# Optimization experiments

Measured on AMD Instinct MI355X. Metric: run time of the kernel, lower is better.

## Reference

```python
import jax, jax.numpy as jnp
import numpy as np

N, D, H, C, E = 16384, 768, 768, 2, 20

def setup_inputs() -> dict:
    key = jax.random.key(0)
    k1, k2, k3, k4, k5, k6 = jax.random.split(key, 6)
    return {
        "embeddings": jax.random.normal(k1, (N, D), dtype=jnp.float32),
        "component_idx": jax.random.randint(k2, (N,), 0, E, dtype=jnp.int64),
        "W1": jax.random.normal(k3, (E, D, H), dtype=jnp.float32) * (1.0 / np.sqrt(D)),
        "b1": jnp.zeros((E, H), dtype=jnp.float32),
        "W2": jax.random.normal(k4, (E, H, C), dtype=jnp.float32) * (1.0 / np.sqrt(H)),
        "b2": jnp.zeros((E, C), dtype=jnp.float32),
    }

def reference(embeddings, component_idx, W1, b1, W2, b2):
    # Each token n goes through expert component_idx[n]:
    #   y = relu(x @ W1[e] + b1[e]) @ W2[e] + b2[e]
    # The torch module's mask/cat/argsort reassembly is mathematically a
    # per-token select of its own expert's output at the original position.
    # Dense-expert formulation (standard jax MoE fallback), then gather.
    h = jax.nn.relu(jnp.einsum('nd,edh->enh', embeddings, W1) + b1[:, None, :])  # [E,N,H]
    y = jnp.einsum('enh,ehc->enc', h, W2) + b2[:, None, :]                        # [E,N,C]
    n_idx = jnp.arange(embeddings.shape[0])
    return y[component_idx, n_idx]  # [N,C]
```

## Files before the change

### kernel.cpp

```cpp
#include <hip/hip_runtime.h>

#define N_D 768
#define N_H 768
#define N_C 2
#define N_E 20
#define MT 128
#define NT 128
#define BK 32
#define KT (N_D / BK)
#define MAX_TILES 160
#define NCOL (N_H / NT)
#define ROWB (N_D * 2)

typedef __attribute__((ext_vector_type(8))) short short8;
typedef __attribute__((ext_vector_type(4))) float f32x4;

__device__ __forceinline__ unsigned short f2bf(float f) {
  unsigned u = __builtin_bit_cast(unsigned, f);
  u += 0x7FFFu + ((u >> 16) & 1u);
  return (unsigned short)(u >> 16);
}

#define GLD_LDS16(gp, lp)                                                        \
  __builtin_amdgcn_global_load_lds(                                              \
      (const __attribute__((address_space(1))) void*)(gp),                       \
      (__attribute__((address_space(3))) void*)(lp), 16, 0, 0)


__global__ __launch_bounds__(256) void k_hist(const int* __restrict__ cidx,
                                              int* __restrict__ counts, int n) {
  __shared__ int lc[N_E];
  if (threadIdx.x < N_E) lc[threadIdx.x] = 0;
  __syncthreads();
  for (int i = blockIdx.x * blockDim.x + threadIdx.x; i < n;
       i += gridDim.x * blockDim.x) {
    int e = cidx[i];
    e = e < 0 ? 0 : (e >= N_E ? N_E - 1 : e);
    atomicAdd(&lc[e], 1);
  }
  __syncthreads();
  if (threadIdx.x < N_E) atomicAdd(&counts[threadIdx.x], lc[threadIdx.x]);
}

__global__ void k_scan(const int* __restrict__ counts, int* __restrict__ offsets,
                       int* __restrict__ cursor, int* __restrict__ tiles,
                       int* __restrict__ numTiles) {
  if (threadIdx.x == 0) {
    int run = 0, t = 0;
    for (int e = 0; e < N_E; ++e) {
      offsets[e] = run;
      cursor[e] = run;
      int nt = (counts[e] + MT - 1) / MT;
      for (int m = 0; m < nt && t < MAX_TILES; ++m) tiles[t++] = (e << 8) | m;
      run += counts[e];
    }
    *numTiles = t;
  }
}


#define SG_TOK 64

__global__ __launch_bounds__(256) void k_scatter_gather(
    const int* __restrict__ cidx, int* __restrict__ cursor,
    int* __restrict__ sorted, const float* __restrict__ emb,
    unsigned short* __restrict__ Xg, int n) {
  __shared__ int lc[N_E];
  __shared__ int lbase[N_E];
  __shared__ int pos_s[SG_TOK];
  const int tid = threadIdx.x;
  const int nb = (n + SG_TOK - 1) / SG_TOK;
  if ((int)blockIdx.x >= nb) {
    ushort4 z = {0, 0, 0, 0};
    ushort4* dst = (ushort4*)(Xg + (size_t)n * N_D);
    for (int k = tid; k < MT * N_D / 4; k += 256) dst[k] = z;
    return;
  }
  const int base_tok = blockIdx.x * SG_TOK;
  if (tid < N_E) lc[tid] = 0;
  __syncthreads();
  const int i = base_tok + tid;
  int e = 0, p = 0;
  if (tid < SG_TOK && i < n) {
    e = cidx[i];
    e = e < 0 ? 0 : (e >= N_E ? N_E - 1 : e);
    p = atomicAdd(&lc[e], 1);
  }
  __syncthreads();
  if (tid < N_E) lbase[tid] = atomicAdd(&cursor[tid], lc[tid]);
  __syncthreads();
  if (tid < SG_TOK) {
    if (i < n) {
      int pos = lbase[e] + p;
      sorted[pos] = i;
      pos_s[tid] = pos;
    } else {
      pos_s[tid] = -1;
    }
  }
  __syncthreads();
  const int wid = tid >> 6, lane = tid & 63;
  int nrows = n - base_tok;
  if (nrows > SG_TOK) nrows = SG_TOK;
  for (int rr = wid; rr < nrows; rr += 4) {
    const float4* s = (const float4*)(emb + (size_t)(base_tok + rr) * N_D);
    ushort4* d = (ushort4*)(Xg + (size_t)pos_s[rr] * N_D);
#pragma unroll
    for (int p2 = 0; p2 < 3; ++p2) {
      float4 v = s[lane + p2 * 64];
      ushort4 o;
      o.x = f2bf(v.x);
      o.y = f2bf(v.y);
      o.z = f2bf(v.z);
      o.w = f2bf(v.w);
      d[lane + p2 * 64] = o;
    }
  }
}


__global__ __launch_bounds__(256) void k_w1_cvt(const float* __restrict__ W1,
                                                unsigned short* __restrict__ W1t) {
  __shared__ float tile[64][65];
  int e = blockIdx.z, h0 = blockIdx.x * 64, d0 = blockIdx.y * 64;
  const float* src = W1 + (size_t)e * N_D * N_H;
  unsigned short* dst = W1t + (size_t)e * N_H * N_D;
  int tx = threadIdx.x & 15, ty = threadIdx.x >> 4;
  for (int s = 0; s < 4; ++s) {
    int d = s * 16 + ty;
    float4 v = *(const float4*)&src[(size_t)(d0 + d) * N_H + h0 + tx * 4];
    tile[d][tx * 4 + 0] = v.x;
    tile[d][tx * 4 + 1] = v.y;
    tile[d][tx * 4 + 2] = v.z;
    tile[d][tx * 4 + 3] = v.w;
  }
  __syncthreads();
  int px = threadIdx.x & 7, py = threadIdx.x >> 3;
  for (int s = 0; s < 2; ++s) {
    int h = s * 32 + py;
    short8 v;
    for (int j = 0; j < 8; ++j)
      v[j] = (short)f2bf(tile[px * 8 + j][h]);
    *(short8*)&dst[(size_t)(h0 + h) * N_D + d0 + px * 8] = v;
  }
}


__global__ __launch_bounds__(256, 2) void k_gemm(
    const unsigned short* __restrict__ Xg, const unsigned short* __restrict__ W1t,
    const float* __restrict__ b1, const float* __restrict__ W2,
    const float* __restrict__ b2, const int* __restrict__ sorted,
    const int* __restrict__ counts, const int* __restrict__ offsets,
    const int* __restrict__ tiles, const int* __restrict__ numTiles,
    float* __restrict__ out) {
  const int nactive = *numTiles * NCOL;
  const int lin = (int)blockIdx.y * NCOL + (int)blockIdx.x;
  if (lin >= nactive) return;
  const int q = nactive >> 3, r = nactive & 7;
  const int c = lin & 7, ii = lin >> 3;
  const int wgid = (c < r ? c * (q + 1) : r * (q + 1) + (c - r) * q) + ii;
  const int tileIdx = wgid / NCOL;
  const int n0 = (wgid - tileIdx * NCOL) * NT;

  const int tv = tiles[tileIdx];
  const int e = tv >> 8;
  const int m0 = (tv & 255) * MT;
  const int off = offsets[e];
  const int cnt_rel = counts[e] - m0;

  __shared__ unsigned short lA[2][MT * BK];
  __shared__ unsigned short lB[2][NT * BK];

  const int tid = threadIdx.x;
  const int wid = tid >> 6, lane = tid & 63;
  const int wm = (wid >> 1) * 64, wn = (wid & 1) * 64;
  const int quad = lane >> 4, lm = lane & 15;

  const int R0 = wid * 32 + lm;
  const char* agp = (const char*)Xg + (size_t)(off + m0 + R0) * ROWB + quad * 16;
  const char* bgp = (const char*)W1t + (size_t)e * N_H * ROWB +
                    (size_t)(n0 + R0) * ROWB + quad * 16;
  unsigned short* lap[2] = {&lA[0][(wid * 32) * BK], &lA[1][(wid * 32) * BK]};
  unsigned short* lbp[2] = {&lB[0][(wid * 32) * BK], &lB[1][(wid * 32) * BK]};

#define ISSUE_BATCH(kk, b)                                                       \
  do {                                                                           \
    const char* a_ = agp + (kk)*64;                                              \
    const char* b_ = bgp + (kk)*64;                                              \
    GLD_LDS16(a_, lap[b]);                                                       \
    GLD_LDS16(a_ + 16 * ROWB, lap[b] + 16 * BK);                                 \
    GLD_LDS16(b_, lbp[b]);                                                       \
    GLD_LDS16(b_ + 16 * ROWB, lbp[b] + 16 * BK);                                 \
  } while (0)

  f32x4 acc[4][4] = {};

  ISSUE_BATCH(0, 0);
  ISSUE_BATCH(1, 1);

  const int fa = quad * 128 + lm * 8;

  for (int kt = 0; kt < KT; ++kt) {
    const int cur = kt & 1;
    asm volatile("s_waitcnt vmcnt(4)\n\ts_barrier" ::: "memory");
    short8 af[4], bfr[4];
    for (int i = 0; i < 4; ++i)
      af[i] = *(const short8*)&lA[cur][((wm >> 4) + i) * 512 + fa];
    for (int j = 0; j < 4; ++j)
      bfr[j] = *(const short8*)&lB[cur][((wn >> 4) + j) * 512 + fa];
    asm volatile("s_waitcnt lgkmcnt(0)\n\ts_barrier" ::: "memory");
    int kk = kt + 2;
    if (kk >= KT) kk -= KT;
    ISSUE_BATCH(kk, cur);
    for (int i = 0; i < 4; ++i)
      for (int j = 0; j < 4; ++j)
        acc[i][j] =
            __builtin_amdgcn_mfma_f32_16x16x32_bf16(af[i], bfr[j], acc[i][j], 0, 0, 0);
  }

  float y0[4][4], y1[4][4];
  for (int i = 0; i < 4; ++i)
    for (int r2 = 0; r2 < 4; ++r2) y0[i][r2] = y1[i][r2] = 0.f;

  for (int j = 0; j < 4; ++j) {
    int col = n0 + wn + j * 16 + lm;
    float bias = b1[e * N_H + col];
    float2 w2 = *(const float2*)&W2[((size_t)e * N_H + col) * N_C];
    for (int i = 0; i < 4; ++i) {
      f32x4 a = acc[i][j];
      for (int r2 = 0; r2 < 4; ++r2) {
        float h = a[r2] + bias;
        h = h > 0.f ? h : 0.f;
        y0[i][r2] += h * w2.x;
        y1[i][r2] += h * w2.y;
      }
    }
  }
  for (int s = 1; s < 16; s <<= 1) {
    for (int i = 0; i < 4; ++i)
      for (int r2 = 0; r2 < 4; ++r2) {
        y0[i][r2] += __shfl_xor(y0[i][r2], s, 64);
        y1[i][r2] += __shfl_xor(y1[i][r2], s, 64);
      }
  }
  if (lm == 0) {
    const bool add_bias = (n0 == 0) && (wn == 0);
    float bb0 = add_bias ? b2[e * N_C + 0] : 0.f;
    float bb1 = add_bias ? b2[e * N_C + 1] : 0.f;
    for (int i = 0; i < 4; ++i) {
      for (int r2 = 0; r2 < 4; ++r2) {
        int mrel = wm + i * 16 + quad * 4 + r2;
        if (mrel < cnt_rel) {
          int token = sorted[off + m0 + mrel];
          atomicAdd(&out[(size_t)token * N_C + 0], y0[i][r2] + bb0);
          atomicAdd(&out[(size_t)token * N_C + 1], y1[i][r2] + bb1);
        }
      }
    }
  }
}


extern "C" void kernel_launch(void* const* d_in, const int* in_sizes, int n_in,
                              void* d_out, int out_size, void* d_ws, size_t ws_size,
                              hipStream_t stream) {
  const float* emb = (const float*)d_in[0];
  const int* cidx = (const int*)d_in[1];
  const float* W1 = (const float*)d_in[2];
  const float* b1 = (const float*)d_in[3];
  const float* W2 = (const float*)d_in[4];
  const float* b2 = (const float*)d_in[5];
  float* out = (float*)d_out;
  const int n = in_sizes[1];

  char* ws = (char*)d_ws;
  int* counts = (int*)ws;
  int* offsets = (int*)(ws + 128);
  int* cursor = (int*)(ws + 256);
  int* numTiles = (int*)(ws + 384);
  int* tiles = (int*)(ws + 512);
  int* sorted = (int*)(ws + 2048);
  size_t sorted_bytes = ((size_t)n * 4 + 255) & ~(size_t)255;
  unsigned short* Xg = (unsigned short*)(ws + 2048 + sorted_bytes);
  int pcap = n + MT;
  unsigned short* W1t = Xg + (size_t)pcap * N_D;

  hipMemsetAsync(d_ws, 0, 2048, stream);
  hipMemsetAsync(d_out, 0, (size_t)out_size * sizeof(float), stream);
  int nb = (n + 255) / 256;
  k_hist<<<nb, 256, 0, stream>>>(cidx, counts, n);
  k_scan<<<1, 64, 0, stream>>>(counts, offsets, cursor, tiles, numTiles);
  int nb64 = (n + SG_TOK - 1) / SG_TOK;
  k_scatter_gather<<<nb64 + 1, 256, 0, stream>>>(cidx, cursor, sorted, emb, Xg, n);
  k_w1_cvt<<<dim3(N_H / 64, N_D / 64, N_E), 256, 0, stream>>>(W1, W1t);
  k_gemm<<<dim3(NCOL, MAX_TILES), 256, 0, stream>>>(
      Xg, W1t, b1, W2, b2, sorted, counts, offsets, tiles, numTiles, out);
}
```

Before: 221.3 us.

## Pre-swizzle A and W1 into MFMA fragment layout and load directly from global

Both the gathered bf16 activations and the converted W1 are now written in a 16-row-group, fragment-major layout, so each lane's MFMA operand is one contiguous 16-byte global load. The GEMM drops LDS staging, double buffering and barriers, and raises the occupancy hint to 3. Expert segments are padded to whole tiles, with a sentinel-filled sorted array that marks padding rows as zeros. This removes the LDS round trip and synchronisation but gives up software pipelining and any reuse of operands across waves, which now re-read them from cache.

New measurement: 220.3 us. Within noise of the previous version (-0.4%).

```diff
diff --git a/kernel.cpp b/kernel.cpp
--- a/kernel.cpp
+++ b/kernel.cpp
@@ -10,7 +10,7 @@
 #define KT (N_D / BK)
 #define MAX_TILES 160
 #define NCOL (N_H / NT)
-#define ROWB (N_D * 2)
+#define GROUP_ELEMS (16 * N_D)
 
 typedef __attribute__((ext_vector_type(8))) short short8;
 typedef __attribute__((ext_vector_type(4))) float f32x4;
@@ -20,11 +20,6 @@
   u += 0x7FFFu + ((u >> 16) & 1u);
   return (unsigned short)(u >> 16);
 }
-
-#define GLD_LDS16(gp, lp)                                                        \
-  __builtin_amdgcn_global_load_lds(                                              \
-      (const __attribute__((address_space(1))) void*)(gp),                       \
-      (__attribute__((address_space(3))) void*)(lp), 16, 0, 0)
 
 
 __global__ __launch_bounds__(256) void k_hist(const int* __restrict__ cidx,
@@ -52,36 +47,23 @@
       cursor[e] = run;
       int nt = (counts[e] + MT - 1) / MT;
       for (int m = 0; m < nt && t < MAX_TILES; ++m) tiles[t++] = (e << 8) | m;
-      run += counts[e];
+      run += nt * MT;
     }
     *numTiles = t;
   }
 }
 
-
-#define SG_TOK 64
-
-__global__ __launch_bounds__(256) void k_scatter_gather(
-    const int* __restrict__ cidx, int* __restrict__ cursor,
-    int* __restrict__ sorted, const float* __restrict__ emb,
-    unsigned short* __restrict__ Xg, int n) {
+__global__ __launch_bounds__(256) void k_scatter(const int* __restrict__ cidx,
+                                                 int* __restrict__ cursor,
+                                                 int* __restrict__ sorted, int n) {
   __shared__ int lc[N_E];
   __shared__ int lbase[N_E];
-  __shared__ int pos_s[SG_TOK];
-  const int tid = threadIdx.x;
-  const int nb = (n + SG_TOK - 1) / SG_TOK;
-  if ((int)blockIdx.x >= nb) {
-    ushort4 z = {0, 0, 0, 0};
-    ushort4* dst = (ushort4*)(Xg + (size_t)n * N_D);
-    for (int k = tid; k < MT * N_D / 4; k += 256) dst[k] = z;
-    return;
-  }
-  const int base_tok = blockIdx.x * SG_TOK;
+  int tid = threadIdx.x;
   if (tid < N_E) lc[tid] = 0;
   __syncthreads();
-  const int i = base_tok + tid;
+  int i = blockIdx.x * blockDim.x + tid;
   int e = 0, p = 0;
-  if (tid < SG_TOK && i < n) {
+  if (i < n) {
     e = cidx[i];
     e = e < 0 ? 0 : (e >= N_E ? N_E - 1 : e);
     p = atomicAdd(&lc[e], 1);
@@ -89,43 +71,48 @@
   __syncthreads();
   if (tid < N_E) lbase[tid] = atomicAdd(&cursor[tid], lc[tid]);
   __syncthreads();
-  if (tid < SG_TOK) {
-    if (i < n) {
-      int pos = lbase[e] + p;
-      sorted[pos] = i;
-      pos_s[tid] = pos;
-    } else {
-      pos_s[tid] = -1;
-    }
-  }
-  __syncthreads();
-  const int wid = tid >> 6, lane = tid & 63;
-  int nrows = n - base_tok;
-  if (nrows > SG_TOK) nrows = SG_TOK;
-  for (int rr = wid; rr < nrows; rr += 4) {
-    const float4* s = (const float4*)(emb + (size_t)(base_tok + rr) * N_D);
-    ushort4* d = (ushort4*)(Xg + (size_t)pos_s[rr] * N_D);
-#pragma unroll
-    for (int p2 = 0; p2 < 3; ++p2) {
-      float4 v = s[lane + p2 * 64];
-      ushort4 o;
-      o.x = f2bf(v.x);
-      o.y = f2bf(v.y);
-      o.z = f2bf(v.z);
-      o.w = f2bf(v.w);
-      d[lane + p2 * 64] = o;
-    }
-  }
-}
-
-
-__global__ __launch_bounds__(256) void k_w1_cvt(const float* __restrict__ W1,
-                                                unsigned short* __restrict__ W1t) {
+  if (i < n) sorted[lbase[e] + p] = i;
+}
+
+
+__global__ __launch_bounds__(256) void k_gather_sw(const float* __restrict__ emb,
+                                                   const int* __restrict__ sorted,
+                                                   unsigned short* __restrict__ Xs) {
+  const int g = blockIdx.x;
+  const int lm = threadIdx.x & 15;
+  const int c0 = threadIdx.x >> 4;
+  const int idx = sorted[g * 16 + lm];
+  const bool valid = idx >= 0;
+  const float* src = emb + (size_t)(valid ? idx : 0) * N_D;
+  unsigned short* dst = Xs + (size_t)g * GROUP_ELEMS + lm * 8;
+#pragma unroll
+  for (int it = 0; it < 6; ++it) {
+    int ch = c0 + 16 * it;
+    short8 v = {};
+    if (valid) {
+      float4 a = *(const float4*)(src + ch * 8);
+      float4 b = *(const float4*)(src + ch * 8 + 4);
+      v[0] = (short)f2bf(a.x);
+      v[1] = (short)f2bf(a.y);
+      v[2] = (short)f2bf(a.z);
+      v[3] = (short)f2bf(a.w);
+      v[4] = (short)f2bf(b.x);
+      v[5] = (short)f2bf(b.y);
+      v[6] = (short)f2bf(b.z);
+      v[7] = (short)f2bf(b.w);
+    }
+    *(short8*)(dst + (size_t)ch * 128) = v;
+  }
+}
+
+
+__global__ __launch_bounds__(256) void k_w1_sw(const float* __restrict__ W1,
+                                               unsigned short* __restrict__ W1s) {
   __shared__ float tile[64][65];
   int e = blockIdx.z, h0 = blockIdx.x * 64, d0 = blockIdx.y * 64;
   const float* src = W1 + (size_t)e * N_D * N_H;
-  unsigned short* dst = W1t + (size_t)e * N_H * N_D;
   int tx = threadIdx.x & 15, ty = threadIdx.x >> 4;
+#pragma unroll
   for (int s = 0; s < 4; ++s) {
     int d = s * 16 + ty;
     float4 v = *(const float4*)&src[(size_t)(d0 + d) * N_H + h0 + tx * 4];
@@ -135,19 +122,25 @@
     tile[d][tx * 4 + 3] = v.w;
   }
   __syncthreads();
-  int px = threadIdx.x & 7, py = threadIdx.x >> 3;
-  for (int s = 0; s < 2; ++s) {
-    int h = s * 32 + py;
+  unsigned short* dst = W1s + (size_t)e * N_H * N_D;
+  int lm = threadIdx.x & 15, u = threadIdx.x >> 4;
+  int gl = u & 3, clb = u >> 2;
+#pragma unroll
+  for (int p = 0; p < 2; ++p) {
+    int cl = clb + 4 * p;
     short8 v;
+#pragma unroll
     for (int j = 0; j < 8; ++j)
-      v[j] = (short)f2bf(tile[px * 8 + j][h]);
-    *(short8*)&dst[(size_t)(h0 + h) * N_D + d0 + px * 8] = v;
-  }
-}
-
-
-__global__ __launch_bounds__(256, 2) void k_gemm(
-    const unsigned short* __restrict__ Xg, const unsigned short* __restrict__ W1t,
+      v[j] = (short)f2bf(tile[cl * 8 + j][gl * 16 + lm]);
+    size_t o = (size_t)(h0 / 16 + gl) * GROUP_ELEMS + (size_t)(d0 / 8 + cl) * 128 +
+               (size_t)lm * 8;
+    *(short8*)(dst + o) = v;
+  }
+}
+
+
+__global__ __launch_bounds__(256, 3) void k_gemm(
+    const unsigned short* __restrict__ Xs, const unsigned short* __restrict__ W1s,
     const float* __restrict__ b1, const float* __restrict__ W2,
     const float* __restrict__ b2, const int* __restrict__ sorted,
     const int* __restrict__ counts, const int* __restrict__ offsets,
@@ -168,54 +161,31 @@
   const int off = offsets[e];
   const int cnt_rel = counts[e] - m0;
 
-  __shared__ unsigned short lA[2][MT * BK];
-  __shared__ unsigned short lB[2][NT * BK];
-
   const int tid = threadIdx.x;
   const int wid = tid >> 6, lane = tid & 63;
   const int wm = (wid >> 1) * 64, wn = (wid & 1) * 64;
   const int quad = lane >> 4, lm = lane & 15;
 
-  const int R0 = wid * 32 + lm;
-  const char* agp = (const char*)Xg + (size_t)(off + m0 + R0) * ROWB + quad * 16;
-  const char* bgp = (const char*)W1t + (size_t)e * N_H * ROWB +
-                    (size_t)(n0 + R0) * ROWB + quad * 16;
-  unsigned short* lap[2] = {&lA[0][(wid * 32) * BK], &lA[1][(wid * 32) * BK]};
-  unsigned short* lbp[2] = {&lB[0][(wid * 32) * BK], &lB[1][(wid * 32) * BK]};
-
-#define ISSUE_BATCH(kk, b)                                                       \
-  do {                                                                           \
-    const char* a_ = agp + (kk)*64;                                              \
-    const char* b_ = bgp + (kk)*64;                                              \
-    GLD_LDS16(a_, lap[b]);                                                       \
-    GLD_LDS16(a_ + 16 * ROWB, lap[b] + 16 * BK);                                 \
-    GLD_LDS16(b_, lbp[b]);                                                       \
-    GLD_LDS16(b_ + 16 * ROWB, lbp[b] + 16 * BK);                                 \
-  } while (0)
+  const unsigned short* Ap = Xs + (size_t)(off + m0 + wm) * N_D + lane * 8;
+  const unsigned short* Bp =
+      W1s + (size_t)e * N_H * N_D + (size_t)(n0 + wn) * N_D + lane * 8;
 
   f32x4 acc[4][4] = {};
-
-  ISSUE_BATCH(0, 0);
-  ISSUE_BATCH(1, 1);
-
-  const int fa = quad * 128 + lm * 8;
-
+#pragma unroll
   for (int kt = 0; kt < KT; ++kt) {
-    const int cur = kt & 1;
-    asm volatile("s_waitcnt vmcnt(4)\n\ts_barrier" ::: "memory");
-    short8 af[4], bfr[4];
+    short8 af[4], bf[4];
+#pragma unroll
     for (int i = 0; i < 4; ++i)
-      af[i] = *(const short8*)&lA[cur][((wm >> 4) + i) * 512 + fa];
+      af[i] = *(const short8*)(Ap + (size_t)i * GROUP_ELEMS + kt * 512);
+#pragma unroll
     for (int j = 0; j < 4; ++j)
-      bfr[j] = *(const short8*)&lB[cur][((wn >> 4) + j) * 512 + fa];
-    asm volatile("s_waitcnt lgkmcnt(0)\n\ts_barrier" ::: "memory");
-    int kk = kt + 2;
-    if (kk >= KT) kk -= KT;
-    ISSUE_BATCH(kk, cur);
+      bf[j] = *(const short8*)(Bp + (size_t)j * GROUP_ELEMS + kt * 512);
+#pragma unroll
     for (int i = 0; i < 4; ++i)
+#pragma unroll
       for (int j = 0; j < 4; ++j)
-        acc[i][j] =
-            __builtin_amdgcn_mfma_f32_16x16x32_bf16(af[i], bfr[j], acc[i][j], 0, 0, 0);
+        acc[i][j] = __builtin_amdgcn_mfma_f32_16x16x32_bf16(af[i], bf[j],
+                                                            acc[i][j], 0, 0, 0);
   }
 
   float y0[4][4], y1[4][4];
@@ -280,19 +250,20 @@
   int* numTiles = (int*)(ws + 384);
   int* tiles = (int*)(ws + 512);
   int* sorted = (int*)(ws + 2048);
-  size_t sorted_bytes = ((size_t)n * 4 + 255) & ~(size_t)255;
-  unsigned short* Xg = (unsigned short*)(ws + 2048 + sorted_bytes);
-  int pcap = n + MT;
-  unsigned short* W1t = Xg + (size_t)pcap * N_D;
+  const int pcap = n + N_E * MT;
+  size_t sorted_bytes = ((size_t)pcap * 4 + 255) & ~(size_t)255;
+  unsigned short* Xs = (unsigned short*)(ws + 2048 + sorted_bytes);
+  unsigned short* W1s = Xs + (size_t)pcap * N_D;
 
   hipMemsetAsync(d_ws, 0, 2048, stream);
+  hipMemsetAsync(sorted, 0xFF, (size_t)pcap * 4, stream);
   hipMemsetAsync(d_out, 0, (size_t)out_size * sizeof(float), stream);
   int nb = (n + 255) / 256;
   k_hist<<<nb, 256, 0, stream>>>(cidx, counts, n);
   k_scan<<<1, 64, 0, stream>>>(counts, offsets, cursor, tiles, numTiles);
-  int nb64 = (n + SG_TOK - 1) / SG_TOK;
-  k_scatter_gather<<<nb64 + 1, 256, 0, stream>>>(cidx, cursor, sorted, emb, Xg, n);
-  k_w1_cvt<<<dim3(N_H / 64, N_D / 64, N_E), 256, 0, stream>>>(W1, W1t);
+  k_scatter<<<nb, 256, 0, stream>>>(cidx, cursor, sorted, n);
+  k_gather_sw<<<pcap / 16, 256, 0, stream>>>(emb, sorted, Xs);
+  k_w1_sw<<<dim3(N_H / 64, N_D / 64, N_E), 256, 0, stream>>>(W1, W1s);
   k_gemm<<<dim3(NCOL, MAX_TILES), 256, 0, stream>>>(
-      Xg, W1t, b1, W2, b2, sorted, counts, offsets, tiles, numTiles, out);
-}
+      Xs, W1s, b1, W2, b2, sorted, counts, offsets, tiles, numTiles, out);
+}
```

## Fuse W1 conversion with histogram, parallelize scan, raise GEMM occupancy bound

Applied to the files above, without the earlier changes.

Merges the W1 transpose/bf16 conversion and the expert histogram into one launch, with the histogram blocks appended after the conversion blocks. This removes one kernel launch and lets the two independent jobs overlap. Replaces the single-thread expert scan with a wavefront shuffle prefix scan. Raises the GEMM launch bound from 2 to 4 blocks per CU, which may force register spills in the GEMM.

Measured after the change: 221.8 us. Within noise of the previous version (+0.2%).

```diff
diff --git a/kernel.cpp b/kernel.cpp
--- a/kernel.cpp
+++ b/kernel.cpp
@@ -11,6 +11,7 @@
 #define MAX_TILES 160
 #define NCOL (N_H / NT)
 #define ROWB (N_D * 2)
+#define W1BLKS (N_E * (N_D / 64) * (N_H / 64))
 
 typedef __attribute__((ext_vector_type(8))) short short8;
 typedef __attribute__((ext_vector_type(4))) float f32x4;
@@ -27,35 +28,83 @@
       (__attribute__((address_space(3))) void*)(lp), 16, 0, 0)
 
 
-__global__ __launch_bounds__(256) void k_hist(const int* __restrict__ cidx,
-                                              int* __restrict__ counts, int n) {
+__global__ __launch_bounds__(256) void k_prep(const float* __restrict__ W1,
+                                              unsigned short* __restrict__ W1t,
+                                              const int* __restrict__ cidx,
+                                              int* __restrict__ counts, int n,
+                                              int hb) {
+  __shared__ float tile[64][65];
   __shared__ int lc[N_E];
-  if (threadIdx.x < N_E) lc[threadIdx.x] = 0;
-  __syncthreads();
-  for (int i = blockIdx.x * blockDim.x + threadIdx.x; i < n;
-       i += gridDim.x * blockDim.x) {
-    int e = cidx[i];
-    e = e < 0 ? 0 : (e >= N_E ? N_E - 1 : e);
-    atomicAdd(&lc[e], 1);
-  }
-  __syncthreads();
-  if (threadIdx.x < N_E) atomicAdd(&counts[threadIdx.x], lc[threadIdx.x]);
-}
+  if ((int)blockIdx.x < W1BLKS) {
+    int bid = blockIdx.x;
+    int e = bid / 144;
+    int rem = bid - e * 144;
+    int h0 = (rem % 12) * 64, d0 = (rem / 12) * 64;
+    const float* src = W1 + (size_t)e * N_D * N_H;
+    unsigned short* dst = W1t + (size_t)e * N_H * N_D;
+    int tx = threadIdx.x & 15, ty = threadIdx.x >> 4;
+#pragma unroll
+    for (int s = 0; s < 4; ++s) {
+      int d = s * 16 + ty;
+      float4 v = *(const float4*)&src[(size_t)(d0 + d) * N_H + h0 + tx * 4];
+      tile[d][tx * 4 + 0] = v.x;
+      tile[d][tx * 4 + 1] = v.y;
+      tile[d][tx * 4 + 2] = v.z;
+      tile[d][tx * 4 + 3] = v.w;
+    }
+    __syncthreads();
+    int px = threadIdx.x & 7, py = threadIdx.x >> 3;
+#pragma unroll
+    for (int s = 0; s < 2; ++s) {
+      int h = s * 32 + py;
+      short8 v;
+#pragma unroll
+      for (int j = 0; j < 8; ++j)
+        v[j] = (short)f2bf(tile[px * 8 + j][h]);
+      *(short8*)&dst[(size_t)(h0 + h) * N_D + d0 + px * 8] = v;
+    }
+  } else {
+    int b = blockIdx.x - W1BLKS;
+    if (threadIdx.x < N_E) lc[threadIdx.x] = 0;
+    __syncthreads();
+    for (int i = b * 256 + threadIdx.x; i < n; i += hb * 256) {
+      int e = cidx[i];
+      e = e < 0 ? 0 : (e >= N_E ? N_E - 1 : e);
+      atomicAdd(&lc[e], 1);
+    }
+    __syncthreads();
+    if (threadIdx.x < N_E) atomicAdd(&counts[threadIdx.x], lc[threadIdx.x]);
+  }
+}
+
 
 __global__ void k_scan(const int* __restrict__ counts, int* __restrict__ offsets,
                        int* __restrict__ cursor, int* __restrict__ tiles,
                        int* __restrict__ numTiles) {
-  if (threadIdx.x == 0) {
-    int run = 0, t = 0;
-    for (int e = 0; e < N_E; ++e) {
-      offsets[e] = run;
-      cursor[e] = run;
-      int nt = (counts[e] + MT - 1) / MT;
-      for (int m = 0; m < nt && t < MAX_TILES; ++m) tiles[t++] = (e << 8) | m;
-      run += counts[e];
-    }
-    *numTiles = t;
-  }
+  int lane = threadIdx.x;
+  int c = (lane < N_E) ? counts[lane] : 0;
+  int nt = (c + MT - 1) / MT;
+  int cs = c, ts = nt;
+#pragma unroll
+  for (int s = 1; s < 32; s <<= 1) {
+    int t1 = __shfl_up(cs, s, 64);
+    int t2 = __shfl_up(ts, s, 64);
+    if (lane >= s) {
+      cs += t1;
+      ts += t2;
+    }
+  }
+  int coff = cs - c;
+  int tbase = ts - nt;
+  if (lane < N_E) {
+    offsets[lane] = coff;
+    cursor[lane] = coff;
+    for (int m = 0; m < nt; ++m) {
+      int t = tbase + m;
+      if (t < MAX_TILES) tiles[t] = (lane << 8) | m;
+    }
+  }
+  if (lane == N_E - 1) *numTiles = ts > MAX_TILES ? MAX_TILES : ts;
 }
 
 
@@ -119,34 +168,7 @@
 }
 
 
-__global__ __launch_bounds__(256) void k_w1_cvt(const float* __restrict__ W1,
-                                                unsigned short* __restrict__ W1t) {
-  __shared__ float tile[64][65];
-  int e = blockIdx.z, h0 = blockIdx.x * 64, d0 = blockIdx.y * 64;
-  const float* src = W1 + (size_t)e * N_D * N_H;
-  unsigned short* dst = W1t + (size_t)e * N_H * N_D;
-  int tx = threadIdx.x & 15, ty = threadIdx.x >> 4;
-  for (int s = 0; s < 4; ++s) {
-    int d = s * 16 + ty;
-    float4 v = *(const float4*)&src[(size_t)(d0 + d) * N_H + h0 + tx * 4];
-    tile[d][tx * 4 + 0] = v.x;
-    tile[d][tx * 4 + 1] = v.y;
-    tile[d][tx * 4 + 2] = v.z;
-    tile[d][tx * 4 + 3] = v.w;
-  }
-  __syncthreads();
-  int px = threadIdx.x & 7, py = threadIdx.x >> 3;
-  for (int s = 0; s < 2; ++s) {
-    int h = s * 32 + py;
-    short8 v;
-    for (int j = 0; j < 8; ++j)
-      v[j] = (short)f2bf(tile[px * 8 + j][h]);
-    *(short8*)&dst[(size_t)(h0 + h) * N_D + d0 + px * 8] = v;
-  }
-}
-
-
-__global__ __launch_bounds__(256, 2) void k_gemm(
+__global__ __launch_bounds__(256, 4) void k_gemm(
     const unsigned short* __restrict__ Xg, const unsigned short* __restrict__ W1t,
     const float* __restrict__ b1, const float* __restrict__ W2,
     const float* __restrict__ b2, const int* __restrict__ sorted,
@@ -287,12 +309,11 @@
 
   hipMemsetAsync(d_ws, 0, 2048, stream);
   hipMemsetAsync(d_out, 0, (size_t)out_size * sizeof(float), stream);
-  int nb = (n + 255) / 256;
-  k_hist<<<nb, 256, 0, stream>>>(cidx, counts, n);
+  int hb = (n + 255) / 256;
+  k_prep<<<W1BLKS + hb, 256, 0, stream>>>(W1, W1t, cidx, counts, n, hb);
   k_scan<<<1, 64, 0, stream>>>(counts, offsets, cursor, tiles, numTiles);
   int nb64 = (n + SG_TOK - 1) / SG_TOK;
   k_scatter_gather<<<nb64 + 1, 256, 0, stream>>>(cidx, cursor, sorted, emb, Xg, n);
-  k_w1_cvt<<<dim3(N_H / 64, N_D / 64, N_E), 256, 0, stream>>>(W1, W1t);
   k_gemm<<<dim3(NCOL, MAX_TILES), 256, 0, stream>>>(
       Xg, W1t, b1, W2, b2, sorted, counts, offsets, tiles, numTiles, out);
 }
```
